# Performance work log

Hardware: AMD Instinct MI355X
Metric: run time of the kernel (lower is better)

Reference implementation:

```python
import jax, jax.numpy as jnp
import numpy as np


def _lecun_tanh(x):
    return 1.7159 * jnp.tanh(0.666 * x)


def _lin_init(k, fan_in, fan_out):
    s = 1.0 / np.sqrt(fan_in)
    kw, kb = jax.random.split(k)
    W = jax.random.uniform(kw, (fan_in, fan_out), minval=-s, maxval=s, dtype=jnp.float32)
    b = jax.random.uniform(kb, (fan_out,), minval=-s, maxval=s, dtype=jnp.float32)
    return W, b


def setup_inputs() -> dict:
    key = jax.random.key(0)
    ks = jax.random.split(key, 8)
    B, T, OBS, H, A = 256, 1024, 32, 128, 8
    Wb, bb = _lin_init(ks[0], OBS + H, H)      # backbone Linear
    Wff1, bff1 = _lin_init(ks[1], H, H)
    Wff2, bff2 = _lin_init(ks[2], H, H)
    Wta, bta = _lin_init(ks[3], H, H)          # time_a
    Wtb, btb = _lin_init(ks[4], H, H)          # time_b
    Wa, ba = _lin_init(ks[5], H, A)            # actor head
    Wc, bc = _lin_init(ks[6], H, 1)            # critic head
    obs = jax.random.normal(ks[7], (B, T, OBS), dtype=jnp.float32)
    return dict(obs=obs, Wb=Wb, bb=bb, Wff1=Wff1, bff1=bff1, Wff2=Wff2, bff2=bff2,
                Wta=Wta, bta=bta, Wtb=Wtb, btb=btb, Wa=Wa, ba=ba, Wc=Wc, bc=bc)


def reference(obs, Wb, bb, Wff1, bff1, Wff2, bff2, Wta, bta, Wtb, btb, Wa, ba, Wc, bc):
    # CfCActorCritic.forward_sequence: CfC (default mode, 1 backbone layer, ts=1)
    # scanned over time, then actor/critic heads on every timestep output.
    B, T, _ = obs.shape
    H = Wff1.shape[0]
    ts = 1.0

    def step(h, x_t):
        z = jnp.concatenate([x_t, h], axis=-1)          # [B, OBS+H]
        z = _lecun_tanh(z @ Wb + bb)                    # backbone MLP
        ff1 = jnp.tanh(z @ Wff1 + bff1)
        ff2 = jnp.tanh(z @ Wff2 + bff2)
        t_interp = jax.nn.sigmoid((z @ Wta + bta) * ts + (z @ Wtb + btb))
        h_new = ff1 * (1.0 - t_interp) + t_interp * ff2
        return h_new, h_new

    h0 = jnp.zeros((B, H), dtype=obs.dtype)
    obs_t = jnp.swapaxes(obs, 0, 1)                     # [T, B, OBS]
    _, ys = jax.lax.scan(step, h0, obs_t)               # ys: [T, B, H]
    out = jnp.swapaxes(ys, 0, 1)                        # [B, T, H]
    mean = out @ Wa + ba                                # [B, T, A]
    value = (out @ Wc + bc).squeeze(-1)                 # [B, T]
    return mean, value
```

## Files before the change

kernel.cpp:

```cpp
#include <hip/hip_runtime.h>


typedef _Float16 half8 __attribute__((ext_vector_type(8)));
typedef float f32x4 __attribute__((ext_vector_type(4)));

#define T_STEPS 1024
#define OBS 32
#define H 128
#define A_DIM 8
#define NW 8
#define NT (NW * 64)
#define ROWS 4
#define NBLK 64

#define ZIN_P 164
#define ZF_P 132

__device__ __forceinline__ float fexp2(float x) { return __builtin_amdgcn_exp2f(x); }
__device__ __forceinline__ float frcp(float x) { return __builtin_amdgcn_rcpf(x); }

__device__ __forceinline__ void sync_lds() {
    __builtin_amdgcn_sched_barrier(0);
    asm volatile("s_waitcnt lgkmcnt(0)" ::: "memory");
    __builtin_amdgcn_s_barrier();
    __builtin_amdgcn_sched_barrier(0);
}

template<bool OFFLOAD>
__global__ void __launch_bounds__(NT) cfc_kernel(
    const float* __restrict__ obs,
    const float* __restrict__ Wb,  const float* __restrict__ bb,
    const float* __restrict__ Wff1, const float* __restrict__ bff1,
    const float* __restrict__ Wff2, const float* __restrict__ bff2,
    const float* __restrict__ Wta, const float* __restrict__ bta,
    const float* __restrict__ Wtb, const float* __restrict__ btb,
    const float* __restrict__ Wa,  const float* __restrict__ ba,
    const float* __restrict__ Wc,  const float* __restrict__ bc,
    float* __restrict__ out_mean, float* __restrict__ out_value,
    _Float16* __restrict__ hist)
{
    const int b0 = blockIdx.x * ROWS;
    const int tid = threadIdx.x;
    const int w = tid >> 6, l = tid & 63;
    const int lo = l & 15, hi = l >> 4;

    __shared__ _Float16 zin[16][ZIN_P];
    __shared__ _Float16 zf[16][ZF_P];

    const int colB = w * 16 + lo;

    half8 Bb[5];
#pragma unroll
    for (int ks = 0; ks < 5; ++ks)
#pragma unroll
        for (int j = 0; j < 8; ++j) {
            int k = ks * 32 + hi * 8 + j;
            Bb[ks][j] = (_Float16)Wb[k * H + colB];
        }
    const float bbv = bb[colB];

    half8 Bg0[4], Bg1[4], Bg2[4];
#pragma unroll
    for (int ks = 0; ks < 4; ++ks)
#pragma unroll
        for (int j = 0; j < 8; ++j) {
            int k = ks * 32 + hi * 8 + j;
            Bg0[ks][j] = (_Float16)Wff1[k * H + colB];
            Bg1[ks][j] = (_Float16)Wff2[k * H + colB];
            Bg2[ks][j] = (_Float16)(Wta[k * H + colB] + Wtb[k * H + colB]);
        }
    const float bg1 = bff1[colB], bg2 = bff2[colB], bg3 = bta[colB] + btb[colB];

    half8 Bh[4];
    float bh = 0.f;
    if (!OFFLOAD && w == 7) {
#pragma unroll
        for (int ks = 0; ks < 4; ++ks)
#pragma unroll
            for (int j = 0; j < 8; ++j) {
                int k = ks * 32 + hi * 8 + j;
                float v = (lo < 8) ? Wa[k * A_DIM + lo] : ((lo == 8) ? Wc[k] : 0.0f);
                Bh[ks][j] = (_Float16)v;
            }
        bh = (lo < 8) ? ba[lo] : ((lo == 8) ? bc[0] : 0.0f);
    }

    for (int i = tid; i < 16 * ZIN_P; i += NT) (&zin[0][0])[i] = (_Float16)0.0f;
    for (int i = tid; i < 16 * ZF_P; i += NT) (&zf[0][0])[i] = (_Float16)0.0f;
    __syncthreads();
    const int rX = (w << 1) | (l >> 5), cX = l & 31;
    if (w < 2) zin[rX][cX] = (_Float16)obs[((size_t)(b0 + rX) * T_STEPS) * OBS + cX];
    __syncthreads();

    float oxA = 0.f, oxB = 0.f;
    if (w < 2) {
        oxA = obs[((size_t)(b0 + rX) * T_STEPS + 1) * OBS + cX];
        oxB = obs[((size_t)(b0 + rX) * T_STEPS + 2) * OBS + cX];
    }

    const int srcl = lo;

    for (int t = 0; t < T_STEPS; ++t) {
        half8 A0 = *(const half8*)&zin[lo][0 * 32 + hi * 8];
        half8 A1 = *(const half8*)&zin[lo][1 * 32 + hi * 8];
        half8 A2 = *(const half8*)&zin[lo][2 * 32 + hi * 8];
        half8 A3 = *(const half8*)&zin[lo][3 * 32 + hi * 8];
        half8 A4 = *(const half8*)&zin[lo][4 * 32 + hi * 8];
        f32x4 az0 = {bbv, bbv, bbv, bbv};
        f32x4 az1 = {0.f, 0.f, 0.f, 0.f};
        az0 = __builtin_amdgcn_mfma_f32_16x16x32_f16(A0, Bb[0], az0, 0, 0, 0);
        az1 = __builtin_amdgcn_mfma_f32_16x16x32_f16(A1, Bb[1], az1, 0, 0, 0);
        az0 = __builtin_amdgcn_mfma_f32_16x16x32_f16(A2, Bb[2], az0, 0, 0, 0);
        az1 = __builtin_amdgcn_mfma_f32_16x16x32_f16(A3, Bb[3], az1, 0, 0, 0);
        az0 = __builtin_amdgcn_mfma_f32_16x16x32_f16(A4, Bb[4], az0, 0, 0, 0);

        if (!OFFLOAD && w == 7 && t > 0) {
            f32x4 acch = {bh, bh, bh, bh};
            acch = __builtin_amdgcn_mfma_f32_16x16x32_f16(A1, Bh[0], acch, 0, 0, 0);
            acch = __builtin_amdgcn_mfma_f32_16x16x32_f16(A2, Bh[1], acch, 0, 0, 0);
            acch = __builtin_amdgcn_mfma_f32_16x16x32_f16(A3, Bh[2], acch, 0, 0, 0);
            acch = __builtin_amdgcn_mfma_f32_16x16x32_f16(A4, Bh[3], acch, 0, 0, 0);
            if (hi == 0 && lo < 9) {
#pragma unroll
                for (int j = 0; j < 4; ++j) {
                    if (lo < 8) out_mean[((size_t)(b0 + j) * T_STEPS + (t - 1)) * A_DIM + lo] = acch[j];
                    else        out_value[(size_t)(b0 + j) * T_STEPS + (t - 1)] = acch[j];
                }
            }
        }

        {
            float s0 = az0[0] + az1[0];
            float s1 = az0[1] + az1[1];
            float s2 = az0[2] + az1[2];
            float s3 = az0[3] + az1[3];
            float p0 = __shfl(s0, srcl);
            float p1 = __shfl(s1, srcl);
            float p2 = __shfl(s2, srcl);
            float p3 = __shfl(s3, srcl);
            float q01 = (hi & 1) ? p1 : p0;
            float q23 = (hi & 1) ? p3 : p2;
            float sv  = (hi & 2) ? q23 : q01;
            float r = frcp(fexp2(1.9216697f * sv) + 1.0f);
            zf[hi][colB] = (_Float16)fmaf(-3.4318f, r, 1.7159f);
        }
        sync_lds();

        half8 Z0 = *(const half8*)&zf[lo][0 * 32 + hi * 8];
        half8 Z1 = *(const half8*)&zf[lo][1 * 32 + hi * 8];
        half8 Z2 = *(const half8*)&zf[lo][2 * 32 + hi * 8];
        half8 Z3 = *(const half8*)&zf[lo][3 * 32 + hi * 8];
        f32x4 a1 = {bg1, bg1, bg1, bg1};
        f32x4 a2 = {bg2, bg2, bg2, bg2};
        f32x4 a3 = {bg3, bg3, bg3, bg3};
        a1 = __builtin_amdgcn_mfma_f32_16x16x32_f16(Z0, Bg0[0], a1, 0, 0, 0);
        a2 = __builtin_amdgcn_mfma_f32_16x16x32_f16(Z0, Bg1[0], a2, 0, 0, 0);
        a3 = __builtin_amdgcn_mfma_f32_16x16x32_f16(Z0, Bg2[0], a3, 0, 0, 0);
        a1 = __builtin_amdgcn_mfma_f32_16x16x32_f16(Z1, Bg0[1], a1, 0, 0, 0);
        a2 = __builtin_amdgcn_mfma_f32_16x16x32_f16(Z1, Bg1[1], a2, 0, 0, 0);
        a3 = __builtin_amdgcn_mfma_f32_16x16x32_f16(Z1, Bg2[1], a3, 0, 0, 0);
        a1 = __builtin_amdgcn_mfma_f32_16x16x32_f16(Z2, Bg0[2], a1, 0, 0, 0);
        a2 = __builtin_amdgcn_mfma_f32_16x16x32_f16(Z2, Bg1[2], a2, 0, 0, 0);
        a3 = __builtin_amdgcn_mfma_f32_16x16x32_f16(Z2, Bg2[2], a3, 0, 0, 0);
        a1 = __builtin_amdgcn_mfma_f32_16x16x32_f16(Z3, Bg0[3], a1, 0, 0, 0);
        a2 = __builtin_amdgcn_mfma_f32_16x16x32_f16(Z3, Bg1[3], a2, 0, 0, 0);
        a3 = __builtin_amdgcn_mfma_f32_16x16x32_f16(Z3, Bg2[3], a3, 0, 0, 0);

        {
            float p0 = __shfl(a1[0], srcl), p1 = __shfl(a1[1], srcl);
            float p2 = __shfl(a1[2], srcl), p3 = __shfl(a1[3], srcl);
            float q01 = (hi & 1) ? p1 : p0, q23 = (hi & 1) ? p3 : p2;
            float v1 = (hi & 2) ? q23 : q01;

            p0 = __shfl(a2[0], srcl); p1 = __shfl(a2[1], srcl);
            p2 = __shfl(a2[2], srcl); p3 = __shfl(a2[3], srcl);
            q01 = (hi & 1) ? p1 : p0; q23 = (hi & 1) ? p3 : p2;
            float v2 = (hi & 2) ? q23 : q01;

            p0 = __shfl(a3[0], srcl); p1 = __shfl(a3[1], srcl);
            p2 = __shfl(a3[2], srcl); p3 = __shfl(a3[3], srcl);
            q01 = (hi & 1) ? p1 : p0; q23 = (hi & 1) ? p3 : p2;
            float v3 = (hi & 2) ? q23 : q01;

            float r1 = frcp(fexp2(2.8853901f * v1) + 1.0f);
            float ff1 = fmaf(-2.0f, r1, 1.0f);
            float r2 = frcp(fexp2(2.8853901f * v2) + 1.0f);
            float ff2 = fmaf(-2.0f, r2, 1.0f);
            float ti = frcp(1.0f + fexp2(-1.44269504f * v3));
            _Float16 hv = (_Float16)(ff1 + ti * (ff2 - ff1));
            zin[hi][32 + colB] = hv;
            if (OFFLOAD)
                hist[((size_t)(b0 + hi) * T_STEPS + t) * H + colB] = hv;
        }

        if (w < 2 && t + 1 < T_STEPS) {
            zin[rX][cX] = (_Float16)oxA;
            oxA = oxB;
            const int tf = t + 3;
            oxB = (tf < T_STEPS) ? obs[((size_t)(b0 + rX) * T_STEPS + tf) * OBS + cX] : 0.0f;
        }
        sync_lds();
    }

    if (OFFLOAD) {
        __syncthreads();
        half8 Bh2[4];
#pragma unroll
        for (int ks = 0; ks < 4; ++ks)
#pragma unroll
            for (int j = 0; j < 8; ++j) {
                int k = ks * 32 + hi * 8 + j;
                float v = (lo < 8) ? Wa[k * A_DIM + lo] : ((lo == 8) ? Wc[k] : 0.0f);
                Bh2[ks][j] = (_Float16)v;
            }
        const float bh2 = (lo < 8) ? ba[lo] : ((lo == 8) ? bc[0] : 0.0f);

        for (int c = w; c < 256; c += NW) {
            const int r = c >> 6;
            const int s0 = (c & 63) << 4;
            const _Float16* hp = hist + ((size_t)(b0 + r) * T_STEPS + (s0 + lo)) * H + hi * 8;
            half8 A0 = *(const half8*)(hp);
            half8 A1 = *(const half8*)(hp + 32);
            half8 A2 = *(const half8*)(hp + 64);
            half8 A3 = *(const half8*)(hp + 96);
            f32x4 acc = {bh2, bh2, bh2, bh2};
            acc = __builtin_amdgcn_mfma_f32_16x16x32_f16(A0, Bh2[0], acc, 0, 0, 0);
            acc = __builtin_amdgcn_mfma_f32_16x16x32_f16(A1, Bh2[1], acc, 0, 0, 0);
            acc = __builtin_amdgcn_mfma_f32_16x16x32_f16(A2, Bh2[2], acc, 0, 0, 0);
            acc = __builtin_amdgcn_mfma_f32_16x16x32_f16(A3, Bh2[3], acc, 0, 0, 0);
            if (lo < 9) {
#pragma unroll
                for (int j = 0; j < 4; ++j) {
                    const int s_ = s0 + hi * 4 + j;
                    if (lo < 8) out_mean[((size_t)(b0 + r) * T_STEPS + s_) * A_DIM + lo] = acc[j];
                    else        out_value[(size_t)(b0 + r) * T_STEPS + s_] = acc[j];
                }
            }
        }
    } else {
        if (w == 7) {
            half8 A1 = *(const half8*)&zin[lo][32 + 0 * 32 + hi * 8];
            half8 A2 = *(const half8*)&zin[lo][32 + 1 * 32 + hi * 8];
            half8 A3 = *(const half8*)&zin[lo][32 + 2 * 32 + hi * 8];
            half8 A4 = *(const half8*)&zin[lo][32 + 3 * 32 + hi * 8];
            f32x4 acch = {bh, bh, bh, bh};
            acch = __builtin_amdgcn_mfma_f32_16x16x32_f16(A1, Bh[0], acch, 0, 0, 0);
            acch = __builtin_amdgcn_mfma_f32_16x16x32_f16(A2, Bh[1], acch, 0, 0, 0);
            acch = __builtin_amdgcn_mfma_f32_16x16x32_f16(A3, Bh[2], acch, 0, 0, 0);
            acch = __builtin_amdgcn_mfma_f32_16x16x32_f16(A4, Bh[3], acch, 0, 0, 0);
            if (hi == 0 && lo < 9) {
#pragma unroll
                for (int j = 0; j < 4; ++j) {
                    if (lo < 8) out_mean[((size_t)(b0 + j) * T_STEPS + (T_STEPS - 1)) * A_DIM + lo] = acch[j];
                    else        out_value[(size_t)(b0 + j) * T_STEPS + (T_STEPS - 1)] = acch[j];
                }
            }
        }
    }
}

extern "C" void kernel_launch(void* const* d_in, const int* in_sizes, int n_in,
                              void* d_out, int out_size, void* d_ws, size_t ws_size,
                              hipStream_t stream) {
    (void)in_sizes; (void)n_in; (void)out_size;
    const float* obs  = (const float*)d_in[0];
    const float* Wb   = (const float*)d_in[1];
    const float* bb   = (const float*)d_in[2];
    const float* Wff1 = (const float*)d_in[3];
    const float* bff1 = (const float*)d_in[4];
    const float* Wff2 = (const float*)d_in[5];
    const float* bff2 = (const float*)d_in[6];
    const float* Wta  = (const float*)d_in[7];
    const float* bta  = (const float*)d_in[8];
    const float* Wtb  = (const float*)d_in[9];
    const float* btb  = (const float*)d_in[10];
    const float* Wa   = (const float*)d_in[11];
    const float* ba   = (const float*)d_in[12];
    const float* Wc   = (const float*)d_in[13];
    const float* bc   = (const float*)d_in[14];
    float* out = (float*)d_out;
    float* out_mean  = out;
    float* out_value = out + (size_t)256 * 1024 * 8;

    const size_t need = (size_t)256 * 1024 * 128 * sizeof(_Float16);
    if (ws_size >= need) {
        cfc_kernel<true><<<dim3(NBLK), dim3(NT), 0, stream>>>(
            obs, Wb, bb, Wff1, bff1, Wff2, bff2, Wta, bta, Wtb, btb,
            Wa, ba, Wc, bc, out_mean, out_value, (_Float16*)d_ws);
    } else {
        cfc_kernel<false><<<dim3(NBLK), dim3(NT), 0, stream>>>(
            obs, Wb, bb, Wff1, bff1, Wff2, bff2, Wta, bta, Wtb, btb,
            Wa, ba, Wc, bc, out_mean, out_value, (_Float16*)d_ws);
    }
}
```

Measured before the change: 1.010 ms.

## Precompute input projection x@Wb before recurrence and shorten per-step dependency chain

Adds a mode that computes the obs-to-hidden projection for all timesteps up front with MFMA and stores it in fp16 workspace. The recurrent loop then needs only four backbone MFMAs on the hidden state and adds a prefetched projection value, removing the per-step obs staging into LDS. It also splits the gate accumulators into two independent chains to reduce MFMA dependency latency. This needs twice the workspace and an extra prologue pass, and the stored projection is rounded to fp16.

```diff
diff --git a/kernel.cpp b/kernel.cpp
--- a/kernel.cpp
+++ b/kernel.cpp
@@ -26,7 +26,7 @@
     __builtin_amdgcn_sched_barrier(0);
 }
 
-template<bool OFFLOAD>
+template<int MODE>
 __global__ void __launch_bounds__(NT) cfc_kernel(
     const float* __restrict__ obs,
     const float* __restrict__ Wb,  const float* __restrict__ bb,
@@ -37,8 +37,9 @@
     const float* __restrict__ Wa,  const float* __restrict__ ba,
     const float* __restrict__ Wc,  const float* __restrict__ bc,
     float* __restrict__ out_mean, float* __restrict__ out_value,
-    _Float16* __restrict__ hist)
+    _Float16* __restrict__ hist, _Float16* __restrict__ pxw)
 {
+    constexpr int HOFF = (MODE == 2) ? 0 : 32;
     const int b0 = blockIdx.x * ROWS;
     const int tid = threadIdx.x;
     const int w = tid >> 6, l = tid & 63;
@@ -50,13 +51,26 @@
     const int colB = w * 16 + lo;
 
     half8 Bb[5];
-#pragma unroll
-    for (int ks = 0; ks < 5; ++ks)
-#pragma unroll
-        for (int j = 0; j < 8; ++j) {
-            int k = ks * 32 + hi * 8 + j;
-            Bb[ks][j] = (_Float16)Wb[k * H + colB];
-        }
+    half8 BbX;
+    if constexpr (MODE == 2) {
+#pragma unroll
+        for (int j = 0; j < 8; ++j) BbX[j] = (_Float16)Wb[(hi * 8 + j) * H + colB];
+#pragma unroll
+        for (int ks = 0; ks < 4; ++ks)
+#pragma unroll
+            for (int j = 0; j < 8; ++j) {
+                int k = (ks + 1) * 32 + hi * 8 + j;
+                Bb[ks][j] = (_Float16)Wb[k * H + colB];
+            }
+    } else {
+#pragma unroll
+        for (int ks = 0; ks < 5; ++ks)
+#pragma unroll
+            for (int j = 0; j < 8; ++j) {
+                int k = ks * 32 + hi * 8 + j;
+                Bb[ks][j] = (_Float16)Wb[k * H + colB];
+            }
+    }
     const float bbv = bb[colB];
 
     half8 Bg0[4], Bg1[4], Bg2[4];
@@ -73,7 +87,7 @@
 
     half8 Bh[4];
     float bh = 0.f;
-    if (!OFFLOAD && w == 7) {
+    if (MODE == 0 && w == 7) {
 #pragma unroll
         for (int ks = 0; ks < 4; ++ks)
 #pragma unroll
@@ -88,56 +102,108 @@
     for (int i = tid; i < 16 * ZIN_P; i += NT) (&zin[0][0])[i] = (_Float16)0.0f;
     for (int i = tid; i < 16 * ZF_P; i += NT) (&zf[0][0])[i] = (_Float16)0.0f;
     __syncthreads();
+
+    float pxU = 0.f, pxV = 0.f;
+    const _Float16* pxL = nullptr;
+    if constexpr (MODE == 2) {
+        for (int r = 0; r < ROWS; ++r) {
+            for (int tc = 0; tc < T_STEPS / 16; ++tc) {
+                const float* xp = obs + ((size_t)(b0 + r) * T_STEPS + tc * 16 + lo) * OBS + hi * 8;
+                float4 xa = *(const float4*)xp;
+                float4 xb = *(const float4*)(xp + 4);
+                half8 Ax;
+                Ax[0] = (_Float16)xa.x; Ax[1] = (_Float16)xa.y;
+                Ax[2] = (_Float16)xa.z; Ax[3] = (_Float16)xa.w;
+                Ax[4] = (_Float16)xb.x; Ax[5] = (_Float16)xb.y;
+                Ax[6] = (_Float16)xb.z; Ax[7] = (_Float16)xb.w;
+                f32x4 acc = {0.f, 0.f, 0.f, 0.f};
+                acc = __builtin_amdgcn_mfma_f32_16x16x32_f16(Ax, BbX, acc, 0, 0, 0);
+#pragma unroll
+                for (int jj = 0; jj < 4; ++jj)
+                    pxw[((size_t)(b0 + r) * T_STEPS + tc * 16 + hi * 4 + jj) * H + colB] = (_Float16)acc[jj];
+            }
+        }
+        __syncthreads();
+        pxL = pxw + ((size_t)(b0 + hi) * T_STEPS) * H + colB;
+        pxU = (float)pxL[0];
+        pxV = (float)pxL[(size_t)1 * H];
+    }
+
     const int rX = (w << 1) | (l >> 5), cX = l & 31;
-    if (w < 2) zin[rX][cX] = (_Float16)obs[((size_t)(b0 + rX) * T_STEPS) * OBS + cX];
-    __syncthreads();
-
     float oxA = 0.f, oxB = 0.f;
-    if (w < 2) {
-        oxA = obs[((size_t)(b0 + rX) * T_STEPS + 1) * OBS + cX];
-        oxB = obs[((size_t)(b0 + rX) * T_STEPS + 2) * OBS + cX];
+    if constexpr (MODE < 2) {
+        if (w < 2) {
+            zin[rX][cX] = (_Float16)obs[((size_t)(b0 + rX) * T_STEPS) * OBS + cX];
+            oxA = obs[((size_t)(b0 + rX) * T_STEPS + 1) * OBS + cX];
+            oxB = obs[((size_t)(b0 + rX) * T_STEPS + 2) * OBS + cX];
+        }
+        __syncthreads();
     }
 
     const int srcl = lo;
 
     for (int t = 0; t < T_STEPS; ++t) {
-        half8 A0 = *(const half8*)&zin[lo][0 * 32 + hi * 8];
-        half8 A1 = *(const half8*)&zin[lo][1 * 32 + hi * 8];
-        half8 A2 = *(const half8*)&zin[lo][2 * 32 + hi * 8];
-        half8 A3 = *(const half8*)&zin[lo][3 * 32 + hi * 8];
-        half8 A4 = *(const half8*)&zin[lo][4 * 32 + hi * 8];
-        f32x4 az0 = {bbv, bbv, bbv, bbv};
-        f32x4 az1 = {0.f, 0.f, 0.f, 0.f};
-        az0 = __builtin_amdgcn_mfma_f32_16x16x32_f16(A0, Bb[0], az0, 0, 0, 0);
-        az1 = __builtin_amdgcn_mfma_f32_16x16x32_f16(A1, Bb[1], az1, 0, 0, 0);
-        az0 = __builtin_amdgcn_mfma_f32_16x16x32_f16(A2, Bb[2], az0, 0, 0, 0);
-        az1 = __builtin_amdgcn_mfma_f32_16x16x32_f16(A3, Bb[3], az1, 0, 0, 0);
-        az0 = __builtin_amdgcn_mfma_f32_16x16x32_f16(A4, Bb[4], az0, 0, 0, 0);
-
-        if (!OFFLOAD && w == 7 && t > 0) {
-            f32x4 acch = {bh, bh, bh, bh};
-            acch = __builtin_amdgcn_mfma_f32_16x16x32_f16(A1, Bh[0], acch, 0, 0, 0);
-            acch = __builtin_amdgcn_mfma_f32_16x16x32_f16(A2, Bh[1], acch, 0, 0, 0);
-            acch = __builtin_amdgcn_mfma_f32_16x16x32_f16(A3, Bh[2], acch, 0, 0, 0);
-            acch = __builtin_amdgcn_mfma_f32_16x16x32_f16(A4, Bh[3], acch, 0, 0, 0);
-            if (hi == 0 && lo < 9) {
-#pragma unroll
-                for (int j = 0; j < 4; ++j) {
-                    if (lo < 8) out_mean[((size_t)(b0 + j) * T_STEPS + (t - 1)) * A_DIM + lo] = acch[j];
-                    else        out_value[(size_t)(b0 + j) * T_STEPS + (t - 1)] = acch[j];
-                }
-            }
-        }
-
-        {
+        if constexpr (MODE == 2) {
+            half8 A1 = *(const half8*)&zin[lo][0 * 32 + hi * 8];
+            half8 A2 = *(const half8*)&zin[lo][1 * 32 + hi * 8];
+            half8 A3 = *(const half8*)&zin[lo][2 * 32 + hi * 8];
+            half8 A4 = *(const half8*)&zin[lo][3 * 32 + hi * 8];
+            f32x4 az0 = {bbv, bbv, bbv, bbv};
+            f32x4 az1 = {0.f, 0.f, 0.f, 0.f};
+            az0 = __builtin_amdgcn_mfma_f32_16x16x32_f16(A1, Bb[0], az0, 0, 0, 0);
+            az1 = __builtin_amdgcn_mfma_f32_16x16x32_f16(A2, Bb[1], az1, 0, 0, 0);
+            az0 = __builtin_amdgcn_mfma_f32_16x16x32_f16(A3, Bb[2], az0, 0, 0, 0);
+            az1 = __builtin_amdgcn_mfma_f32_16x16x32_f16(A4, Bb[3], az1, 0, 0, 0);
+
             float s0 = az0[0] + az1[0];
             float s1 = az0[1] + az1[1];
             float s2 = az0[2] + az1[2];
             float s3 = az0[3] + az1[3];
-            float p0 = __shfl(s0, srcl);
-            float p1 = __shfl(s1, srcl);
-            float p2 = __shfl(s2, srcl);
-            float p3 = __shfl(s3, srcl);
+            float p0 = __shfl(s0, srcl), p1 = __shfl(s1, srcl);
+            float p2 = __shfl(s2, srcl), p3 = __shfl(s3, srcl);
+            float q01 = (hi & 1) ? p1 : p0;
+            float q23 = (hi & 1) ? p3 : p2;
+            float sv  = ((hi & 2) ? q23 : q01) + pxU;
+            float r = frcp(fexp2(1.9216697f * sv) + 1.0f);
+            zf[hi][colB] = (_Float16)fmaf(-3.4318f, r, 1.7159f);
+
+            pxU = pxV;
+            pxV = (t + 2 < T_STEPS) ? (float)pxL[(size_t)(t + 2) * H] : 0.0f;
+        } else {
+            half8 A0 = *(const half8*)&zin[lo][0 * 32 + hi * 8];
+            half8 A1 = *(const half8*)&zin[lo][1 * 32 + hi * 8];
+            half8 A2 = *(const half8*)&zin[lo][2 * 32 + hi * 8];
+            half8 A3 = *(const half8*)&zin[lo][3 * 32 + hi * 8];
+            half8 A4 = *(const half8*)&zin[lo][4 * 32 + hi * 8];
+            f32x4 az0 = {bbv, bbv, bbv, bbv};
+            f32x4 az1 = {0.f, 0.f, 0.f, 0.f};
+            az0 = __builtin_amdgcn_mfma_f32_16x16x32_f16(A0, Bb[0], az0, 0, 0, 0);
+            az1 = __builtin_amdgcn_mfma_f32_16x16x32_f16(A1, Bb[1], az1, 0, 0, 0);
+            az0 = __builtin_amdgcn_mfma_f32_16x16x32_f16(A2, Bb[2], az0, 0, 0, 0);
+            az1 = __builtin_amdgcn_mfma_f32_16x16x32_f16(A3, Bb[3], az1, 0, 0, 0);
+            az0 = __builtin_amdgcn_mfma_f32_16x16x32_f16(A4, Bb[4], az0, 0, 0, 0);
+
+            if (MODE == 0 && w == 7 && t > 0) {
+                f32x4 acch = {bh, bh, bh, bh};
+                acch = __builtin_amdgcn_mfma_f32_16x16x32_f16(A1, Bh[0], acch, 0, 0, 0);
+                acch = __builtin_amdgcn_mfma_f32_16x16x32_f16(A2, Bh[1], acch, 0, 0, 0);
+                acch = __builtin_amdgcn_mfma_f32_16x16x32_f16(A3, Bh[2], acch, 0, 0, 0);
+                acch = __builtin_amdgcn_mfma_f32_16x16x32_f16(A4, Bh[3], acch, 0, 0, 0);
+                if (hi == 0 && lo < 9) {
+#pragma unroll
+                    for (int j = 0; j < 4; ++j) {
+                        if (lo < 8) out_mean[((size_t)(b0 + j) * T_STEPS + (t - 1)) * A_DIM + lo] = acch[j];
+                        else        out_value[(size_t)(b0 + j) * T_STEPS + (t - 1)] = acch[j];
+                    }
+                }
+            }
+
+            float s0 = az0[0] + az1[0];
+            float s1 = az0[1] + az1[1];
+            float s2 = az0[2] + az1[2];
+            float s3 = az0[3] + az1[3];
+            float p0 = __shfl(s0, srcl), p1 = __shfl(s1, srcl);
+            float p2 = __shfl(s2, srcl), p3 = __shfl(s3, srcl);
             float q01 = (hi & 1) ? p1 : p0;
             float q23 = (hi & 1) ? p3 : p2;
             float sv  = (hi & 2) ? q23 : q01;
@@ -150,59 +216,92 @@
         half8 Z1 = *(const half8*)&zf[lo][1 * 32 + hi * 8];
         half8 Z2 = *(const half8*)&zf[lo][2 * 32 + hi * 8];
         half8 Z3 = *(const half8*)&zf[lo][3 * 32 + hi * 8];
-        f32x4 a1 = {bg1, bg1, bg1, bg1};
-        f32x4 a2 = {bg2, bg2, bg2, bg2};
-        f32x4 a3 = {bg3, bg3, bg3, bg3};
-        a1 = __builtin_amdgcn_mfma_f32_16x16x32_f16(Z0, Bg0[0], a1, 0, 0, 0);
-        a2 = __builtin_amdgcn_mfma_f32_16x16x32_f16(Z0, Bg1[0], a2, 0, 0, 0);
-        a3 = __builtin_amdgcn_mfma_f32_16x16x32_f16(Z0, Bg2[0], a3, 0, 0, 0);
-        a1 = __builtin_amdgcn_mfma_f32_16x16x32_f16(Z1, Bg0[1], a1, 0, 0, 0);
-        a2 = __builtin_amdgcn_mfma_f32_16x16x32_f16(Z1, Bg1[1], a2, 0, 0, 0);
-        a3 = __builtin_amdgcn_mfma_f32_16x16x32_f16(Z1, Bg2[1], a3, 0, 0, 0);
-        a1 = __builtin_amdgcn_mfma_f32_16x16x32_f16(Z2, Bg0[2], a1, 0, 0, 0);
-        a2 = __builtin_amdgcn_mfma_f32_16x16x32_f16(Z2, Bg1[2], a2, 0, 0, 0);
-        a3 = __builtin_amdgcn_mfma_f32_16x16x32_f16(Z2, Bg2[2], a3, 0, 0, 0);
-        a1 = __builtin_amdgcn_mfma_f32_16x16x32_f16(Z3, Bg0[3], a1, 0, 0, 0);
-        a2 = __builtin_amdgcn_mfma_f32_16x16x32_f16(Z3, Bg1[3], a2, 0, 0, 0);
-        a3 = __builtin_amdgcn_mfma_f32_16x16x32_f16(Z3, Bg2[3], a3, 0, 0, 0);
-
-        {
+
+        float v1, v2, v3;
+        if constexpr (MODE == 2) {
+            f32x4 a1a = {bg1, bg1, bg1, bg1}, a1b = {0.f, 0.f, 0.f, 0.f};
+            f32x4 a2a = {bg2, bg2, bg2, bg2}, a2b = {0.f, 0.f, 0.f, 0.f};
+            f32x4 a3a = {bg3, bg3, bg3, bg3}, a3b = {0.f, 0.f, 0.f, 0.f};
+            a1a = __builtin_amdgcn_mfma_f32_16x16x32_f16(Z0, Bg0[0], a1a, 0, 0, 0);
+            a2a = __builtin_amdgcn_mfma_f32_16x16x32_f16(Z0, Bg1[0], a2a, 0, 0, 0);
+            a3a = __builtin_amdgcn_mfma_f32_16x16x32_f16(Z0, Bg2[0], a3a, 0, 0, 0);
+            a1b = __builtin_amdgcn_mfma_f32_16x16x32_f16(Z1, Bg0[1], a1b, 0, 0, 0);
+            a2b = __builtin_amdgcn_mfma_f32_16x16x32_f16(Z1, Bg1[1], a2b, 0, 0, 0);
+            a3b = __builtin_amdgcn_mfma_f32_16x16x32_f16(Z1, Bg2[1], a3b, 0, 0, 0);
+            a1a = __builtin_amdgcn_mfma_f32_16x16x32_f16(Z2, Bg0[2], a1a, 0, 0, 0);
+            a2a = __builtin_amdgcn_mfma_f32_16x16x32_f16(Z2, Bg1[2], a2a, 0, 0, 0);
+            a3a = __builtin_amdgcn_mfma_f32_16x16x32_f16(Z2, Bg2[2], a3a, 0, 0, 0);
+            a1b = __builtin_amdgcn_mfma_f32_16x16x32_f16(Z3, Bg0[3], a1b, 0, 0, 0);
+            a2b = __builtin_amdgcn_mfma_f32_16x16x32_f16(Z3, Bg1[3], a2b, 0, 0, 0);
+            a3b = __builtin_amdgcn_mfma_f32_16x16x32_f16(Z3, Bg2[3], a3b, 0, 0, 0);
+
+            float p0 = __shfl(a1a[0] + a1b[0], srcl), p1 = __shfl(a1a[1] + a1b[1], srcl);
+            float p2 = __shfl(a1a[2] + a1b[2], srcl), p3 = __shfl(a1a[3] + a1b[3], srcl);
+            float q01 = (hi & 1) ? p1 : p0, q23 = (hi & 1) ? p3 : p2;
+            v1 = (hi & 2) ? q23 : q01;
+            p0 = __shfl(a2a[0] + a2b[0], srcl); p1 = __shfl(a2a[1] + a2b[1], srcl);
+            p2 = __shfl(a2a[2] + a2b[2], srcl); p3 = __shfl(a2a[3] + a2b[3], srcl);
+            q01 = (hi & 1) ? p1 : p0; q23 = (hi & 1) ? p3 : p2;
+            v2 = (hi & 2) ? q23 : q01;
+            p0 = __shfl(a3a[0] + a3b[0], srcl); p1 = __shfl(a3a[1] + a3b[1], srcl);
+            p2 = __shfl(a3a[2] + a3b[2], srcl); p3 = __shfl(a3a[3] + a3b[3], srcl);
+            q01 = (hi & 1) ? p1 : p0; q23 = (hi & 1) ? p3 : p2;
+            v3 = (hi & 2) ? q23 : q01;
+        } else {
+            f32x4 a1 = {bg1, bg1, bg1, bg1};
+            f32x4 a2 = {bg2, bg2, bg2, bg2};
+            f32x4 a3 = {bg3, bg3, bg3, bg3};
+            a1 = __builtin_amdgcn_mfma_f32_16x16x32_f16(Z0, Bg0[0], a1, 0, 0, 0);
+            a2 = __builtin_amdgcn_mfma_f32_16x16x32_f16(Z0, Bg1[0], a2, 0, 0, 0);
+            a3 = __builtin_amdgcn_mfma_f32_16x16x32_f16(Z0, Bg2[0], a3, 0, 0, 0);
+            a1 = __builtin_amdgcn_mfma_f32_16x16x32_f16(Z1, Bg0[1], a1, 0, 0, 0);
+            a2 = __builtin_amdgcn_mfma_f32_16x16x32_f16(Z1, Bg1[1], a2, 0, 0, 0);
+            a3 = __builtin_amdgcn_mfma_f32_16x16x32_f16(Z1, Bg2[1], a3, 0, 0, 0);
+            a1 = __builtin_amdgcn_mfma_f32_16x16x32_f16(Z2, Bg0[2], a1, 0, 0, 0);
+            a2 = __builtin_amdgcn_mfma_f32_16x16x32_f16(Z2, Bg1[2], a2, 0, 0, 0);
+            a3 = __builtin_amdgcn_mfma_f32_16x16x32_f16(Z2, Bg2[2], a3, 0, 0, 0);
+            a1 = __builtin_amdgcn_mfma_f32_16x16x32_f16(Z3, Bg0[3], a1, 0, 0, 0);
+            a2 = __builtin_amdgcn_mfma_f32_16x16x32_f16(Z3, Bg1[3], a2, 0, 0, 0);
+            a3 = __builtin_amdgcn_mfma_f32_16x16x32_f16(Z3, Bg2[3], a3, 0, 0, 0);
+
             float p0 = __shfl(a1[0], srcl), p1 = __shfl(a1[1], srcl);
             float p2 = __shfl(a1[2], srcl), p3 = __shfl(a1[3], srcl);
             float q01 = (hi & 1) ? p1 : p0, q23 = (hi & 1) ? p3 : p2;
-            float v1 = (hi & 2) ? q23 : q01;
-
+            v1 = (hi & 2) ? q23 : q01;
             p0 = __shfl(a2[0], srcl); p1 = __shfl(a2[1], srcl);
             p2 = __shfl(a2[2], srcl); p3 = __shfl(a2[3], srcl);
             q01 = (hi & 1) ? p1 : p0; q23 = (hi & 1) ? p3 : p2;
-            float v2 = (hi & 2) ? q23 : q01;
-
+            v2 = (hi & 2) ? q23 : q01;
             p0 = __shfl(a3[0], srcl); p1 = __shfl(a3[1], srcl);
             p2 = __shfl(a3[2], srcl); p3 = __shfl(a3[3], srcl);
             q01 = (hi & 1) ? p1 : p0; q23 = (hi & 1) ? p3 : p2;
-            float v3 = (hi & 2) ? q23 : q01;
-
+            v3 = (hi & 2) ? q23 : q01;
+        }
+
+        {
             float r1 = frcp(fexp2(2.8853901f * v1) + 1.0f);
             float ff1 = fmaf(-2.0f, r1, 1.0f);
             float r2 = frcp(fexp2(2.8853901f * v2) + 1.0f);
             float ff2 = fmaf(-2.0f, r2, 1.0f);
             float ti = frcp(1.0f + fexp2(-1.44269504f * v3));
             _Float16 hv = (_Float16)(ff1 + ti * (ff2 - ff1));
-            zin[hi][32 + colB] = hv;
-            if (OFFLOAD)
+            zin[hi][HOFF + colB] = hv;
+            if (MODE >= 1)
                 hist[((size_t)(b0 + hi) * T_STEPS + t) * H + colB] = hv;
         }
 
-        if (w < 2 && t + 1 < T_STEPS) {
-            zin[rX][cX] = (_Float16)oxA;
-            oxA = oxB;
-            const int tf = t + 3;
-            oxB = (tf < T_STEPS) ? obs[((size_t)(b0 + rX) * T_STEPS + tf) * OBS + cX] : 0.0f;
+        if constexpr (MODE < 2) {
+            if (w < 2 && t + 1 < T_STEPS) {
+                zin[rX][cX] = (_Float16)oxA;
+                oxA = oxB;
+                const int tf = t + 3;
+                oxB = (tf < T_STEPS) ? obs[((size_t)(b0 + rX) * T_STEPS + tf) * OBS + cX] : 0.0f;
+            }
         }
         sync_lds();
     }
 
-    if (OFFLOAD) {
+    if constexpr (MODE >= 1) {
         __syncthreads();
         half8 Bh2[4];
 #pragma unroll
@@ -282,14 +381,21 @@
     float* out_mean  = out;
     float* out_value = out + (size_t)256 * 1024 * 8;
 
-    const size_t need = (size_t)256 * 1024 * 128 * sizeof(_Float16);
-    if (ws_size >= need) {
-        cfc_kernel<true><<<dim3(NBLK), dim3(NT), 0, stream>>>(
+    const size_t one = (size_t)256 * 1024 * 128 * sizeof(_Float16);
+    _Float16* hist = (_Float16*)d_ws;
+    _Float16* pxw  = hist + (size_t)256 * 1024 * 128;
+
+    if (ws_size >= 2 * one) {
+        cfc_kernel<2><<<dim3(NBLK), dim3(NT), 0, stream>>>(
             obs, Wb, bb, Wff1, bff1, Wff2, bff2, Wta, bta, Wtb, btb,
-            Wa, ba, Wc, bc, out_mean, out_value, (_Float16*)d_ws);
+            Wa, ba, Wc, bc, out_mean, out_value, hist, pxw);
+    } else if (ws_size >= one) {
+        cfc_kernel<1><<<dim3(NBLK), dim3(NT), 0, stream>>>(
+            obs, Wb, bb, Wff1, bff1, Wff2, bff2, Wta, bta, Wtb, btb,
+            Wa, ba, Wc, bc, out_mean, out_value, hist, pxw);
     } else {
-        cfc_kernel<false><<<dim3(NBLK), dim3(NT), 0, stream>>>(
+        cfc_kernel<0><<<dim3(NBLK), dim3(NT), 0, stream>>>(
             obs, Wb, bb, Wff1, bff1, Wff2, bff2, Wta, bta, Wtb, btb,
-            Wa, ba, Wc, bc, out_mean, out_value, (_Float16*)d_ws);
+            Wa, ba, Wc, bc, out_mean, out_value, hist, pxw);
     }
 }
```

Result: slower. 1.158 ms (+14.6%).
